# Optimization experiments

Measured on AMD Instinct MI355X. Metric: run time of the kernel, lower is better.

## Reference

```python
import jax, jax.numpy as jnp
import numpy as np

K, N = 64, 4096

def setup_inputs() -> dict:
    key = jax.random.key(0)
    k1, k2 = jax.random.split(key)
    zs = jax.random.uniform(k1, (K, N), dtype=jnp.float32)        # K candidate schedules
    X = jax.random.uniform(k2, (N, N), dtype=jnp.float32)         # channel gain matrix
    var_noise = jnp.asarray(1.0, dtype=jnp.float32)
    return {"zs": zs, "X": X, "var_noise": var_noise}

def reference(zs, X, var_noise):
    # Original per-sample math: all_info[i,j] = z[j]*X[i,j]
    #   numerators   = diag(all_info) = z * diag(X)
    #   denominators = row_sum(all_info) - numerators = X @ z - numerators
    # Batched over K zs: one GEMM instead of K O(n^2) elementwise products.
    row_sums = jnp.einsum('kn,in->ki', zs, X)       # [K, N] = (X @ z_k)_i
    numerators = zs * jnp.diagonal(X)[None, :]      # [K, N]
    denominators = row_sums - numerators            # [K, N]
    per_sample = -jnp.sum(numerators / (var_noise + denominators), axis=1)  # [K]
    return jnp.sum(per_sample) / zs.shape[0]
```

## Files before the change

### kernel.cpp

```cpp
#include <hip/hip_runtime.h>

#define N_DIM 4096

typedef float f4  __attribute__((ext_vector_type(4)));
typedef short s8v __attribute__((ext_vector_type(8)));

#if defined(__has_builtin)
#if __has_builtin(__builtin_amdgcn_cvt_pk_bf16_f32)
#define HAVE_CVT_PK 1
#endif
#endif

static __device__ __forceinline__ unsigned int f2bf_pair(float lo, float hi) {
#ifdef HAVE_CVT_PK
    typedef __bf16 bf2 __attribute__((ext_vector_type(2)));
    bf2 p = __builtin_amdgcn_cvt_pk_bf16_f32(lo, hi);
    return __builtin_bit_cast(unsigned int, p);
#else
    unsigned int ul = __builtin_bit_cast(unsigned int, lo);
    unsigned int uh = __builtin_bit_cast(unsigned int, hi);
    ul = ul + 0x7fffu + ((ul >> 16) & 1u);
    uh = uh + 0x7fffu + ((uh >> 16) & 1u);
    return (uh & 0xffff0000u) | (ul >> 16);
#endif
}

static __device__ __forceinline__ s8v cvt8(f4 a, f4 b) {
    unsigned int u4[4] = { f2bf_pair(a[0], a[1]), f2bf_pair(a[2], a[3]),
                           f2bf_pair(b[0], b[1]), f2bf_pair(b[2], b[3]) };
    return __builtin_bit_cast(s8v, u4);
}

#define MFMA(a, b, c) __builtin_amdgcn_mfma_f32_16x16x32_bf16((a), (b), (c), 0, 0, 0)

__global__ __launch_bounds__(512) void fused_kernel(
    const float* __restrict__ zs, const float* __restrict__ X,
    const float* __restrict__ varp, float* __restrict__ bsum) {
    __shared__ s8v zsP[2][1024];
    __shared__ s8v xP [2][256];
    __shared__ f4  accx[256];
    __shared__ float wred[8];

    const int tid  = threadIdx.x;
    const int lane = tid & 63;
    const int w    = tid >> 6;
    const int kh   = w & 3;
    const int nh   = w >> 2;
    const int i0   = blockIdx.x * 16;

    const int zr  = tid >> 3;
    const int zc  = tid & 7;
    const int zi0 = zr * 16 + (zc ^ (zr & 7));
    const int zi1 = zi0 + 8;
    const float* gz = zs + (size_t)zr * N_DIM + zc * 8;

    const int xr  = (tid & 255) >> 4;
    const int xc  = tid & 15;
    const int xi  = xr * 16 + (xc ^ (xr & 7));
    const float* gx = X + (size_t)(i0 + xr) * N_DIM + xc * 8;

    const int arow = kh * 16 + (lane & 15);
    const int brow = lane & 15;
    const int cb0  = nh * 8 + (lane >> 4);
    const int ai0  = arow * 16 + ((cb0    ) ^ (lane & 7));
    const int ai1  = arow * 16 + ((cb0 + 4) ^ (lane & 7));
    const int bi0  = brow * 16 + ((cb0    ) ^ (lane & 7));
    const int bi1  = brow * 16 + ((cb0 + 4) ^ (lane & 7));

    f4 rzA0, rzA1, rzA2, rzA3, rzB0, rzB1, rzB2, rzB3;
    f4 rxA0 = {}, rxA1 = {}, rxB0 = {}, rxB1 = {};
    rzA0 = *(const f4*)(gz);       rzA1 = *(const f4*)(gz + 4);
    rzA2 = *(const f4*)(gz + 64);  rzA3 = *(const f4*)(gz + 68);
    rzB0 = *(const f4*)(gz + 128); rzB1 = *(const f4*)(gz + 132);
    rzB2 = *(const f4*)(gz + 192); rzB3 = *(const f4*)(gz + 196);
    if (tid < 256) {
        rxA0 = *(const f4*)(gx);       rxA1 = *(const f4*)(gx + 4);
        rxB0 = *(const f4*)(gx + 128); rxB1 = *(const f4*)(gx + 132);
    }

    f4 acc = {};

#define STEP(L, BI, T)                                                        \
    {                                                                         \
        s8v pz0 = cvt8(rz##L##0, rz##L##1);                                   \
        s8v pz1 = cvt8(rz##L##2, rz##L##3);                                   \
        s8v px0 = {};                                                         \
        if (tid < 256) px0 = cvt8(rx##L##0, rx##L##1);                        \
        if ((T) < 30) {      \
            const float* z = gz + ((T) + 2) * 128;                            \
            rz##L##0 = *(const f4*)(z);      rz##L##1 = *(const f4*)(z + 4);  \
            rz##L##2 = *(const f4*)(z + 64); rz##L##3 = *(const f4*)(z + 68); \
            if (tid < 256) {                                                  \
                const float* x = gx + ((T) + 2) * 128;                        \
                rx##L##0 = *(const f4*)(x);  rx##L##1 = *(const f4*)(x + 4);  \
            }                                                                 \
        }                                                                     \
        zsP[BI][zi0] = pz0; zsP[BI][zi1] = pz1;                               \
        if (tid < 256) xP[BI][xi] = px0;                                      \
        asm volatile("s_waitcnt lgkmcnt(0)\n\ts_barrier" ::: "memory");       \
        s8v a0 = zsP[BI][ai0], b0 = xP[BI][bi0];                              \
        s8v a1 = zsP[BI][ai1], b1 = xP[BI][bi1];                              \
        acc = MFMA(a0, b0, acc);                                              \
        acc = MFMA(a1, b1, acc);                                              \
    }

    for (int m = 0; m < 16; ++m) {
        STEP(A, 0, 2 * m)
        STEP(B, 1, 2 * m + 1)
    }
#undef STEP

    if (nh == 1) accx[kh * 64 + lane] = acc;
    __syncthreads();

    float vsum = 0.f;
    if (nh == 0) {
        f4 o = accx[kh * 64 + lane];
        const int   i   = i0 + (lane & 15);
        const float dg  = X[(size_t)i * (N_DIM + 1)];
        const float var = varp[0];
        #pragma unroll
        for (int r = 0; r < 4; ++r) {
            const int   k   = kh * 16 + (lane >> 4) * 4 + r;
            const float num = zs[(size_t)k * N_DIM + i] * dg;
            const float den = (acc[r] + o[r]) - num;
            vsum += num / (var + den);
        }
    }
    #pragma unroll
    for (int off = 32; off >= 1; off >>= 1) vsum += __shfl_down(vsum, off);
    if (lane == 0) wred[w] = vsum;
    __syncthreads();
    if (tid == 0) bsum[blockIdx.x] = wred[0] + wred[1] + wred[2] + wred[3];
}

__global__ __launch_bounds__(256) void reduce_kernel(
    const float* __restrict__ bsum, float* __restrict__ out) {
    const int tid = threadIdx.x;
    float v = bsum[tid];
    #pragma unroll
    for (int off = 32; off >= 1; off >>= 1) v += __shfl_down(v, off);
    __shared__ float s4[4];
    if ((tid & 63) == 0) s4[tid >> 6] = v;
    __syncthreads();
    if (tid == 0) *out = -(s4[0] + s4[1] + s4[2] + s4[3]) * (1.0f / 64.0f);
}

extern "C" void kernel_launch(void* const* d_in, const int* in_sizes, int n_in,
                              void* d_out, int out_size, void* d_ws, size_t ws_size,
                              hipStream_t stream) {
    const float* zs   = (const float*)d_in[0];
    const float* X    = (const float*)d_in[1];
    const float* varp = (const float*)d_in[2];
    float* out  = (float*)d_out;
    float* bsum = (float*)d_ws;

    hipLaunchKernelGGL(fused_kernel, dim3(256), dim3(512), 0, stream,
                       zs, X, varp, bsum);
    hipLaunchKernelGGL(reduce_kernel, dim3(1), dim3(256), 0, stream,
                       bsum, out);
}
```

Before: 113.6 us.

## Split GEMM reduction dimension across two blocks and move epilogue to separate kernel

The GEMM kernel now splits the 4096-long reduction dimension into two halves, launching a 2x256 grid so twice as many blocks stream X concurrently. Each block writes its partial 64x16 result to workspace. A new epilogue kernel sums the two partials, computes the SINR terms and atomically accumulates into the output, which the GEMM kernel zeroes. This is meant to fill more CUs on a 256-CU device and shorten each block's serial loop, at the cost of a partials round-trip through global memory and a float atomic with nondeterministic summation order.

```diff
diff --git a/kernel.cpp b/kernel.cpp
--- a/kernel.cpp
+++ b/kernel.cpp
@@ -33,31 +33,33 @@
 
 #define MFMA(a, b, c) __builtin_amdgcn_mfma_f32_16x16x32_bf16((a), (b), (c), 0, 0, 0)
 
-__global__ __launch_bounds__(512) void fused_kernel(
+__global__ __launch_bounds__(512) void gemm_kernel(
     const float* __restrict__ zs, const float* __restrict__ X,
-    const float* __restrict__ varp, float* __restrict__ bsum) {
+    float* __restrict__ part, float* __restrict__ out) {
     __shared__ s8v zsP[2][1024];
     __shared__ s8v xP [2][256];
     __shared__ f4  accx[256];
-    __shared__ float wred[8];
 
     const int tid  = threadIdx.x;
     const int lane = tid & 63;
     const int w    = tid >> 6;
     const int kh   = w & 3;
     const int nh   = w >> 2;
-    const int i0   = blockIdx.x * 16;
+    const int nb   = blockIdx.x * 2048;
+    const int i0   = blockIdx.y * 16;
+
+    if (blockIdx.x == 0 && blockIdx.y == 0 && tid == 0) *out = 0.f;
 
     const int zr  = tid >> 3;
     const int zc  = tid & 7;
     const int zi0 = zr * 16 + (zc ^ (zr & 7));
     const int zi1 = zi0 + 8;
-    const float* gz = zs + (size_t)zr * N_DIM + zc * 8;
+    const float* gz = zs + (size_t)zr * N_DIM + nb + zc * 8;
 
     const int xr  = (tid & 255) >> 4;
     const int xc  = tid & 15;
     const int xi  = xr * 16 + (xc ^ (xr & 7));
-    const float* gx = X + (size_t)(i0 + xr) * N_DIM + xc * 8;
+    const float* gx = X + (size_t)(i0 + xr) * N_DIM + nb + xc * 8;
 
     const int arow = kh * 16 + (lane & 15);
     const int brow = lane & 15;
@@ -86,7 +88,7 @@
         s8v pz1 = cvt8(rz##L##2, rz##L##3);                                   \
         s8v px0 = {};                                                         \
         if (tid < 256) px0 = cvt8(rx##L##0, rx##L##1);                        \
-        if ((T) < 30) {      \
+        if ((T) < 14) {      \
             const float* z = gz + ((T) + 2) * 128;                            \
             rz##L##0 = *(const f4*)(z);      rz##L##1 = *(const f4*)(z + 4);  \
             rz##L##2 = *(const f4*)(z + 64); rz##L##3 = *(const f4*)(z + 68); \
@@ -104,7 +106,7 @@
         acc = MFMA(a1, b1, acc);                                              \
     }
 
-    for (int m = 0; m < 16; ++m) {
+    for (int m = 0; m < 8; ++m) {
         STEP(A, 0, 2 * m)
         STEP(B, 1, 2 * m + 1)
     }
@@ -112,38 +114,48 @@
 
     if (nh == 1) accx[kh * 64 + lane] = acc;
     __syncthreads();
+    if (nh == 0) {
+        f4 o = accx[tid];
+        f4 s; s[0] = acc[0] + o[0]; s[1] = acc[1] + o[1];
+              s[2] = acc[2] + o[2]; s[3] = acc[3] + o[3];
+        ((f4*)part)[(blockIdx.y * 2 + blockIdx.x) * 256 + tid] = s;
+    }
+}
+
+__global__ __launch_bounds__(256) void epilogue_kernel(
+    const float* __restrict__ part, const float* __restrict__ zs,
+    const float* __restrict__ X, const float* __restrict__ varp,
+    float* __restrict__ out) {
+    const int tid  = threadIdx.x;
+    const int lane = tid & 63;
+    const int w    = tid >> 6;
+    const int it   = blockIdx.x;
+    const f4* pp   = (const f4*)part;
+
+    f4 a = pp[(it * 2 + 0) * 256 + tid];
+    f4 b = pp[(it * 2 + 1) * 256 + tid];
+    f4 s; s[0] = a[0] + b[0]; s[1] = a[1] + b[1];
+          s[2] = a[2] + b[2]; s[3] = a[3] + b[3];
+
+    const int   i   = it * 16 + (lane & 15);
+    const int   k0  = w * 16 + (lane >> 4) * 4;
+    const float dg  = X[(size_t)i * (N_DIM + 1)];
+    const float var = varp[0];
 
     float vsum = 0.f;
-    if (nh == 0) {
-        f4 o = accx[kh * 64 + lane];
-        const int   i   = i0 + (lane & 15);
-        const float dg  = X[(size_t)i * (N_DIM + 1)];
-        const float var = varp[0];
-        #pragma unroll
-        for (int r = 0; r < 4; ++r) {
-            const int   k   = kh * 16 + (lane >> 4) * 4 + r;
-            const float num = zs[(size_t)k * N_DIM + i] * dg;
-            const float den = (acc[r] + o[r]) - num;
-            vsum += num / (var + den);
-        }
+    #pragma unroll
+    for (int r = 0; r < 4; ++r) {
+        const float num = zs[(size_t)(k0 + r) * N_DIM + i] * dg;
+        const float den = s[r] - num;
+        vsum += num / (var + den);
     }
     #pragma unroll
     for (int off = 32; off >= 1; off >>= 1) vsum += __shfl_down(vsum, off);
+    __shared__ float wred[4];
     if (lane == 0) wred[w] = vsum;
     __syncthreads();
-    if (tid == 0) bsum[blockIdx.x] = wred[0] + wred[1] + wred[2] + wred[3];
-}
-
-__global__ __launch_bounds__(256) void reduce_kernel(
-    const float* __restrict__ bsum, float* __restrict__ out) {
-    const int tid = threadIdx.x;
-    float v = bsum[tid];
-    #pragma unroll
-    for (int off = 32; off >= 1; off >>= 1) v += __shfl_down(v, off);
-    __shared__ float s4[4];
-    if ((tid & 63) == 0) s4[tid >> 6] = v;
-    __syncthreads();
-    if (tid == 0) *out = -(s4[0] + s4[1] + s4[2] + s4[3]) * (1.0f / 64.0f);
+    if (tid == 0)
+        atomicAdd(out, -(wred[0] + wred[1] + wred[2] + wred[3]) * (1.0f / 64.0f));
 }
 
 extern "C" void kernel_launch(void* const* d_in, const int* in_sizes, int n_in,
@@ -153,10 +165,10 @@
     const float* X    = (const float*)d_in[1];
     const float* varp = (const float*)d_in[2];
     float* out  = (float*)d_out;
-    float* bsum = (float*)d_ws;
+    float* part = (float*)d_ws;
 
-    hipLaunchKernelGGL(fused_kernel, dim3(256), dim3(512), 0, stream,
-                       zs, X, varp, bsum);
-    hipLaunchKernelGGL(reduce_kernel, dim3(1), dim3(256), 0, stream,
-                       bsum, out);
+    hipLaunchKernelGGL(gemm_kernel, dim3(2, 256), dim3(512), 0, stream,
+                       zs, X, part, out);
+    hipLaunchKernelGGL(epilogue_kernel, dim3(256), dim3(256), 0, stream,
+                       part, zs, X, varp, out);
 }
```

Result: no change. 112.3 us (-1.2%).
